# Optimization experiments

Measured on AMD Instinct MI355X. Metric: run time of the kernel, lower is better.

Reference implementation:

```python
import jax, jax.numpy as jnp
import numpy as np

NEAR = 0.01          # near-plane clip for camera-space depth
BLUR = 0.3           # 2D covariance dilation used by 3DGS/gsplat rasterizers
MAX_ALPHA = 0.999    # alpha clamp used by 3DGS/gsplat


def _quat_to_rotmat(q):
    # q: [N,4] normalized (w, x, y, z)
    w, x, y, z = q[:, 0], q[:, 1], q[:, 2], q[:, 3]
    return jnp.stack([
        jnp.stack([1 - 2 * (y * y + z * z), 2 * (x * y - w * z), 2 * (x * z + w * y)], -1),
        jnp.stack([2 * (x * y + w * z), 1 - 2 * (x * x + z * z), 2 * (y * z - w * x)], -1),
        jnp.stack([2 * (x * z - w * y), 2 * (y * z + w * x), 1 - 2 * (x * x + y * y)], -1),
    ], -2)  # [N,3,3]


def _render_one(viewmat, K, means, quats_n, scales, opacities, colors, width, height):
    # --- 3D covariance: Sigma = R diag(s^2) R^T ---
    R = _quat_to_rotmat(quats_n)                      # [N,3,3]
    M = R * scales[:, None, :]                        # scale columns
    cov3d = jnp.einsum('nij,nkj->nik', M, M)          # [N,3,3]

    # --- project means to camera / image ---
    Rcw, tvec = viewmat[:3, :3], viewmat[:3, 3]
    tc = means @ Rcw.T + tvec                         # [N,3] camera-space
    tz = tc[:, 2]
    fx, fy, cx, cy = K[0, 0], K[1, 1], K[0, 2], K[1, 2]
    tz_safe = jnp.where(tz > NEAR, tz, NEAR)
    inv_z = 1.0 / tz_safe
    mean2d = jnp.stack([fx * tc[:, 0] * inv_z + cx,
                        fy * tc[:, 1] * inv_z + cy], -1)  # [N,2]

    # --- EWA splatting: cov2d = J W Sigma W^T J^T + blur*I ---
    zeros = jnp.zeros_like(inv_z)
    J = jnp.stack([
        jnp.stack([fx * inv_z, zeros, -fx * tc[:, 0] * inv_z * inv_z], -1),
        jnp.stack([zeros, fy * inv_z, -fy * tc[:, 1] * inv_z * inv_z], -1),
    ], -2)                                            # [N,2,3]
    cov_cam = jnp.einsum('ij,njk,lk->nil', Rcw, cov3d, Rcw)
    cov2d = jnp.einsum('nij,njk,nlk->nil', J, cov_cam, J)
    a = cov2d[:, 0, 0] + BLUR
    c = cov2d[:, 1, 1] + BLUR
    b = cov2d[:, 0, 1]
    det = a * c - b * b
    valid = (tz > NEAR) & (det > 1e-12)
    det_s = jnp.where(valid, det, 1.0)
    ia, ib, ic = c / det_s, -b / det_s, a / det_s     # conic (inverse cov2d)

    # --- depth sort (front to back) ---
    order = jnp.argsort(tz)
    mean2d, ia, ib, ic = mean2d[order], ia[order], ib[order], ic[order]
    opac_s, colors_s, valid_s = opacities[order], colors[order], valid[order]

    # --- per-pixel gaussian evaluation (pixel centers at +0.5) ---
    px = jnp.arange(width, dtype=mean2d.dtype) + 0.5   # [W]
    py = jnp.arange(height, dtype=mean2d.dtype) + 0.5  # [H]
    dx = px[:, None] - mean2d[None, :, 0]              # [W,N]
    dy = py[:, None] - mean2d[None, :, 1]              # [H,N]
    quad = (ia * dx * dx)[None, :, :] \
         + 2.0 * ib * dx[None, :, :] * dy[:, None, :] \
         + (ic * dy * dy)[:, None, :]                  # [H,W,N]
    alpha = opac_s * jnp.exp(-0.5 * quad)
    alpha = jnp.where(valid_s, jnp.minimum(alpha, MAX_ALPHA), 0.0)

    # --- front-to-back alpha compositing ---
    Tinc = jnp.cumprod(1.0 - alpha, axis=-1)
    Texc = jnp.concatenate([jnp.ones_like(Tinc[..., :1]), Tinc[..., :-1]], -1)
    w = alpha * Texc                                   # [H,W,N]
    return jnp.einsum('hwn,nc->hwc', w, colors_s)      # [H,W,3]


def reference(viewmats, Ks, means, quats, log_scales, opacity_logits, color_logits, width, height):
    # parameter activations (GaussianSplat.activated_parameters)
    quats_n = quats / jnp.linalg.norm(quats, axis=-1, keepdims=True)
    scales = jnp.exp(log_scales)
    opac = jax.nn.sigmoid(opacity_logits)
    colors = jax.nn.sigmoid(color_logits)
    render = lambda vm, K: _render_one(vm, K, means, quats_n, scales, opac, colors, width, height)
    return jax.vmap(render)(viewmats, Ks)  # [C,H,W,3]


def setup_inputs() -> dict:
    key = jax.random.key(0)
    k1, k2, k3 = jax.random.split(key, 3)
    N = 1024
    means = jax.random.normal(k1, (N, 3), dtype=jnp.float32) * 0.1
    quats = jnp.concatenate([jnp.ones((N, 1), jnp.float32),
                             jnp.zeros((N, 3), jnp.float32)], -1)
    quats = quats + 0.1 * jax.random.normal(k3, (N, 4), dtype=jnp.float32)
    log_scales = jnp.full((N, 3), -2.3, dtype=jnp.float32)
    opacity_logits = jnp.full((N,), -1.0, dtype=jnp.float32)
    color_logits = jax.random.normal(k2, (N, 3), dtype=jnp.float32)

    def look(angle):
        c, s = np.cos(angle), np.sin(angle)
        vm = np.eye(4, dtype=np.float32)
        vm[:3, :3] = np.array([[c, 0, -s], [0, 1, 0], [s, 0, c]], np.float32)
        vm[:3, 3] = np.array([0, 0, 2.5], np.float32)
        return vm

    viewmats = jnp.asarray(np.stack([look(0.0), look(0.4)]))
    K = np.array([[128.0, 0, 64.0], [0, 128.0, 64.0], [0, 0, 1.0]], np.float32)
    Ks = jnp.asarray(np.stack([K, K]))
    return {"viewmats": viewmats, "Ks": Ks, "means": means, "quats": quats,
            "log_scales": log_scales, "opacity_logits": opacity_logits,
            "color_logits": color_logits, "width": 128, "height": 128}
```

## Files before the change

kernel.cpp:

```cpp
#include <hip/hip_runtime.h>
#include <hip/hip_fp16.h>
#include <math.h>

#define NEARP 0.01f
#define BLUR 0.3f
#define MAX_ALPHA 0.999f
#define TILE 16
#define NSEG 16
#define QCUT 32.0f

__device__ __forceinline__ float sigmoidf_(float x) {
    return 1.0f / (1.0f + expf(-x));
}

__global__ void gs_preprocess(const float* __restrict__ viewmats,
                              const float* __restrict__ Ks,
                              const float* __restrict__ means,
                              const float* __restrict__ quats,
                              const float* __restrict__ log_scales,
                              const float* __restrict__ opac_logits,
                              const float* __restrict__ color_logits,
                              float4* __restrict__ ubbox,
                              float4* __restrict__ upay,
                              float* __restrict__ tz_out,
                              int N, int C) {
    int idx = blockIdx.x * blockDim.x + threadIdx.x;
    if (idx >= N * C) return;
    int c = idx / N;
    int n = idx - c * N;

    float qw = quats[n * 4 + 0], qx = quats[n * 4 + 1];
    float qy = quats[n * 4 + 2], qz = quats[n * 4 + 3];
    float qn = rsqrtf(qw * qw + qx * qx + qy * qy + qz * qz);
    float w = qw * qn, x = qx * qn, y = qy * qn, z = qz * qn;
    float R00 = 1.0f - 2.0f * (y * y + z * z), R01 = 2.0f * (x * y - w * z), R02 = 2.0f * (x * z + w * y);
    float R10 = 2.0f * (x * y + w * z), R11 = 1.0f - 2.0f * (x * x + z * z), R12 = 2.0f * (y * z - w * x);
    float R20 = 2.0f * (x * z - w * y), R21 = 2.0f * (y * z + w * x), R22 = 1.0f - 2.0f * (x * x + y * y);

    float s0 = expf(log_scales[n * 3 + 0]);
    float s1 = expf(log_scales[n * 3 + 1]);
    float s2 = expf(log_scales[n * 3 + 2]);

    float M00 = R00 * s0, M01 = R01 * s1, M02 = R02 * s2;
    float M10 = R10 * s0, M11 = R11 * s1, M12 = R12 * s2;
    float M20 = R20 * s0, M21 = R21 * s1, M22 = R22 * s2;
    float C00 = M00 * M00 + M01 * M01 + M02 * M02;
    float C01 = M00 * M10 + M01 * M11 + M02 * M12;
    float C02 = M00 * M20 + M01 * M21 + M02 * M22;
    float C11 = M10 * M10 + M11 * M11 + M12 * M12;
    float C12 = M10 * M20 + M11 * M21 + M12 * M22;
    float C22 = M20 * M20 + M21 * M21 + M22 * M22;

    const float* vm = viewmats + c * 16;
    float V00 = vm[0], V01 = vm[1], V02 = vm[2], T0 = vm[3];
    float V10 = vm[4], V11 = vm[5], V12 = vm[6], T1 = vm[7];
    float V20 = vm[8], V21 = vm[9], V22 = vm[10], T2 = vm[11];
    float mex = means[n * 3 + 0], mey = means[n * 3 + 1], mez = means[n * 3 + 2];
    float tx = V00 * mex + V01 * mey + V02 * mez + T0;
    float ty = V10 * mex + V11 * mey + V12 * mez + T1;
    float tz = V20 * mex + V21 * mey + V22 * mez + T2;

    float fx = Ks[c * 9 + 0], fy = Ks[c * 9 + 4], cx = Ks[c * 9 + 2], cy = Ks[c * 9 + 5];
    float tzs = (tz > NEARP) ? tz : NEARP;
    float iz = 1.0f / tzs;
    float m2x = fx * tx * iz + cx;
    float m2y = fy * ty * iz + cy;

    float A00 = V00 * C00 + V01 * C01 + V02 * C02;
    float A01 = V00 * C01 + V01 * C11 + V02 * C12;
    float A02 = V00 * C02 + V01 * C12 + V02 * C22;
    float A10 = V10 * C00 + V11 * C01 + V12 * C02;
    float A11 = V10 * C01 + V11 * C11 + V12 * C12;
    float A12 = V10 * C02 + V11 * C12 + V12 * C22;
    float A20 = V20 * C00 + V21 * C01 + V22 * C02;
    float A21 = V20 * C01 + V21 * C11 + V22 * C12;
    float A22 = V20 * C02 + V21 * C12 + V22 * C22;
    float S00 = A00 * V00 + A01 * V01 + A02 * V02;
    float S01 = A00 * V10 + A01 * V11 + A02 * V12;
    float S02 = A00 * V20 + A01 * V21 + A02 * V22;
    float S11 = A10 * V10 + A11 * V11 + A12 * V12;
    float S12 = A10 * V20 + A11 * V21 + A12 * V22;
    float S22 = A20 * V20 + A21 * V21 + A22 * V22;

    float J00 = fx * iz, J02 = -fx * tx * iz * iz;
    float J11 = fy * iz, J12 = -fy * ty * iz * iz;

    float c2_00 = J00 * J00 * S00 + 2.0f * J00 * J02 * S02 + J02 * J02 * S22;
    float c2_01 = J00 * J11 * S01 + J00 * J12 * S02 + J02 * J11 * S12 + J02 * J12 * S22;
    float c2_11 = J11 * J11 * S11 + 2.0f * J11 * J12 * S12 + J12 * J12 * S22;

    float a = c2_00 + BLUR;
    float cc = c2_11 + BLUR;
    float b = c2_01;
    float det = a * cc - b * b;
    bool valid = (tz > NEARP) && (det > 1e-12f);

    float ia, ib, ic, op, r;
    if (valid) {
        float inv = 1.0f / det;
        ia = cc * inv;
        ib = -b * inv;
        ic = a * inv;
        op = sigmoidf_(opac_logits[n]);
        float lmax = 0.5f * (a + cc) + sqrtf(0.25f * (a - cc) * (a - cc) + b * b);
        r = sqrtf(QCUT * lmax);
    } else {
        ia = 0.0f; ib = 0.0f; ic = 0.0f; op = 0.0f;
        r = -1.0f;
    }
    float cr = sigmoidf_(color_logits[n * 3 + 0]);
    float cg = sigmoidf_(color_logits[n * 3 + 1]);
    float cb = sigmoidf_(color_logits[n * 3 + 2]);

    const float KQ = 0.721347520444482f;
    float iap = -KQ * ia;
    float ibp = -2.0f * KQ * ib;
    float icp = -KQ * ic;

    union { __half2 h; float f; } pk;
    pk.h = __floats2half2_rn(cr, cg);

    int gi = c * N + n;
    ubbox[gi] = make_float4(m2x, m2y, r, 0.0f);
    upay[(size_t)gi * 2 + 0] = make_float4(m2x, m2y, iap, ibp);
    upay[(size_t)gi * 2 + 1] = make_float4(icp, op, pk.f, cb);
    tz_out[gi] = tz;
}

__global__ void gs_sort_wave(const float4* __restrict__ ubbox,
                             const float4* __restrict__ upay,
                             const float* __restrict__ tzin,
                             float4* __restrict__ sbbox,
                             float4* __restrict__ spay,
                             int N, int C) {
    int gtid = blockIdx.x * blockDim.x + threadIdx.x;
    int wid = gtid >> 6;
    int lane = gtid & 63;
    if (wid >= C * N) return;
    int c = wid / N;
    int i = wid - c * N;
    const float* tzc = tzin + (size_t)c * N;
    float ti = tzc[i];
    int rank = 0;
    for (int j = lane; j < N; j += 64) {
        float tj = tzc[j];
        rank += (int)((tj < ti) || (tj == ti && j < i));
    }
#pragma unroll
    for (int off = 1; off < 64; off <<= 1)
        rank += __shfl_xor(rank, off, 64);
    int src = c * N + i;
    int dst = c * N + rank;
    if (lane == 0) sbbox[dst] = ubbox[src];
    if (lane < 2) spay[(size_t)dst * 2 + lane] = upay[(size_t)src * 2 + lane];
}

__global__ void gs_tilebuild(const float4* __restrict__ sbbox,
                             int* __restrict__ tcount,
                             int* __restrict__ tlist,
                             int N, int C, int tilesx, int tilesy) {
    int gtid = blockIdx.x * blockDim.x + threadIdx.x;
    int wid = gtid >> 6;
    int lane = gtid & 63;
    int T = tilesx * tilesy;
    if (wid >= C * T) return;
    int c = wid / T;
    int t = wid - c * T;
    float x0 = (float)((t % tilesx) * TILE);
    float y0 = (float)((t / tilesx) * TILE);
    float x1 = x0 + (float)TILE;
    float y1 = y0 + (float)TILE;

    const float4* bb = sbbox + (size_t)c * N;
    int* lst = tlist + (size_t)wid * N;
    int cnt = 0;
    for (int base = 0; base < N; base += 64) {
        int g = base + lane;
        bool pred = false;
        if (g < N) {
            float4 b = bb[g];
            pred = (b.z >= 0.0f) &&
                   (b.x - b.z <= x1) && (b.x + b.z >= x0) &&
                   (b.y - b.z <= y1) && (b.y + b.z >= y0);
        }
        unsigned long long bal = __ballot(pred);
        if (pred) {
            int off = __popcll(bal & ((1ull << lane) - 1ull));
            lst[cnt + off] = g;
        }
        cnt += (int)__popcll(bal);
    }
    if (lane == 0) tcount[wid] = cnt;
}

__global__ void __launch_bounds__(256) gs_render_tile(const float4* __restrict__ spay,
                                                      const int* __restrict__ tcount,
                                                      const int* __restrict__ tlist,
                                                      float4* __restrict__ partial,
                                                      int N, int W, int H,
                                                      int tilesx, int nseg) {
    int zc = blockIdx.z;
    int c = zc / nseg;
    int s = zc - c * nseg;
    int t = blockIdx.y * tilesx + blockIdx.x;
    int T = tilesx * ((H + TILE - 1) / TILE);
    int wid = c * T + t;

    int cnt = tcount[wid];
    int L = (cnt + nseg - 1) / nseg;
    int k0 = s * L;
    int k1 = min(cnt, k0 + L);

    int lx = threadIdx.x % TILE;
    int ly = threadIdx.x / TILE;
    int x = blockIdx.x * TILE + lx;
    int y = blockIdx.y * TILE + ly;
    float px = (float)x + 0.5f;
    float py = (float)y + 0.5f;

    float Tr = 1.0f, accr = 0.0f, accg = 0.0f, accb = 0.0f;
    const int* lst = tlist + (size_t)wid * N;
    const float4* pay = spay + (size_t)c * N * 2;

#pragma unroll 4
    for (int k = k0; k < k1; k++) {
        int idx = lst[k];
        float4 f0 = pay[(size_t)idx * 2 + 0];
        float4 f1 = pay[(size_t)idx * 2 + 1];
        float dx = px - f0.x;
        float dy = py - f0.y;
        float quad = dx * (f0.z * dx + f0.w * dy) + f1.x * dy * dy;
        float alpha = f1.y * exp2f(quad);
        alpha = fminf(alpha, MAX_ALPHA);
        union { float f; __half2 h; } pk; pk.f = f1.z;
        float wgt = alpha * Tr;
        accr += wgt * __low2float(pk.h);
        accg += wgt * __high2float(pk.h);
        accb += wgt * f1.w;
        Tr *= (1.0f - alpha);
    }
    if (x < W && y < H) {
        partial[((size_t)zc * H + y) * W + x] = make_float4(accr, accg, accb, Tr);
    }
}

__global__ void gs_combine(const float4* __restrict__ partial,
                           float* __restrict__ out,
                           int W, int H, int nseg, int C) {
    int pid = blockIdx.x * blockDim.x + threadIdx.x;
    int PIX = W * H;
    if (pid >= C * PIX) return;
    int c = pid / PIX;
    int p = pid - c * PIX;
    float T = 1.0f, r = 0.0f, g = 0.0f, b = 0.0f;
    for (int s = 0; s < nseg; s++) {
        float4 ps = partial[(size_t)(c * nseg + s) * PIX + p];
        r += T * ps.x;
        g += T * ps.y;
        b += T * ps.z;
        T *= ps.w;
    }
    size_t o = (size_t)pid * 3;
    out[o + 0] = r;
    out[o + 1] = g;
    out[o + 2] = b;
}

extern "C" void kernel_launch(void* const* d_in, const int* in_sizes, int n_in,
                              void* d_out, int out_size, void* d_ws, size_t ws_size,
                              hipStream_t stream) {
    const float* viewmats = (const float*)d_in[0];
    const float* Ks = (const float*)d_in[1];
    const float* means = (const float*)d_in[2];
    const float* quats = (const float*)d_in[3];
    const float* log_scales = (const float*)d_in[4];
    const float* opac_logits = (const float*)d_in[5];
    const float* color_logits = (const float*)d_in[6];
    float* out = (float*)d_out;

    int N = in_sizes[2] / 3;
    int C = in_sizes[0] / 16;
    int pix = out_size / (C * 3);
    int W = (int)(sqrt((double)pix) + 0.5);
    int H = pix / W;
    int tilesx = (W + TILE - 1) / TILE;
    int tilesy = (H + TILE - 1) / TILE;
    int T = tilesx * tilesy;
    int nseg = NSEG;

    float4* ubbox = (float4*)d_ws;
    float4* sbbox = ubbox + (size_t)C * N;
    float4* upay  = sbbox + (size_t)C * N;
    float4* spay  = upay + (size_t)C * N * 2;
    float4* partial = spay + (size_t)C * N * 2;
    float*  tzbuf = (float*)(partial + (size_t)C * nseg * pix);
    int*    tcount = (int*)(tzbuf + (size_t)C * N);
    int*    tlist  = tcount + (size_t)C * T;

    int total = C * N;
    gs_preprocess<<<(total + 255) / 256, 256, 0, stream>>>(
        viewmats, Ks, means, quats, log_scales, opac_logits, color_logits,
        ubbox, upay, tzbuf, N, C);

    gs_sort_wave<<<(total * 64 + 255) / 256, 256, 0, stream>>>(
        ubbox, upay, tzbuf, sbbox, spay, N, C);

    gs_tilebuild<<<(C * T * 64 + 255) / 256, 256, 0, stream>>>(
        sbbox, tcount, tlist, N, C, tilesx, tilesy);

    dim3 grid(tilesx, tilesy, C * nseg);
    gs_render_tile<<<grid, 256, 0, stream>>>(
        spay, tcount, tlist, partial, N, W, H, tilesx, nseg);

    int cp = C * W * H;
    gs_combine<<<(cp + 255) / 256, 256, 0, stream>>>(partial, out, W, H, nseg, C);
}
```

Baseline: 114.4 us.

## Fuse tile binning into render kernel and drop per-tile gaussian lists

Removes the separate tile-build kernel and its per-tile index lists. Each render block now scans its own fixed range of 64-gaussian chunks of the depth-sorted array, tests bbox overlap with a wave ballot, and blends only the overlapping gaussians. Partial results are stored in a tile-major layout, and the combine kernel maps them back to pixel order. This saves one launch and the list write and read traffic. In exchange every block repeats the overlap test for its chunk range, and splitting by chunk count instead of by per-tile hit count can leave the work across segments uneven.

```diff
diff --git a/kernel.cpp b/kernel.cpp
--- a/kernel.cpp
+++ b/kernel.cpp
@@ -155,27 +155,33 @@
     if (lane < 2) spay[(size_t)dst * 2 + lane] = upay[(size_t)src * 2 + lane];
 }
 
-__global__ void gs_tilebuild(const float4* __restrict__ sbbox,
-                             int* __restrict__ tcount,
-                             int* __restrict__ tlist,
-                             int N, int C, int tilesx, int tilesy) {
-    int gtid = blockIdx.x * blockDim.x + threadIdx.x;
-    int wid = gtid >> 6;
-    int lane = gtid & 63;
-    int T = tilesx * tilesy;
-    if (wid >= C * T) return;
-    int c = wid / T;
-    int t = wid - c * T;
-    float x0 = (float)((t % tilesx) * TILE);
-    float y0 = (float)((t / tilesx) * TILE);
+__global__ void __launch_bounds__(256) gs_render_seg(const float4* __restrict__ sbbox,
+                                                     const float4* __restrict__ spay,
+                                                     float4* __restrict__ partial,
+                                                     int N, int W, int H,
+                                                     int tilesx, int nseg, int cps) {
+    int zc = blockIdx.z;
+    int c = zc / nseg;
+    int s = zc - c * nseg;
+    int nchunk = (N + 63) >> 6;
+    int v0 = s * cps;
+    int v1 = min(nchunk, v0 + cps);
+
+    float x0 = (float)(blockIdx.x * TILE);
+    float y0 = (float)(blockIdx.y * TILE);
     float x1 = x0 + (float)TILE;
     float y1 = y0 + (float)TILE;
 
+    int lane = threadIdx.x & 63;
+    float px = x0 + (float)(threadIdx.x & 15) + 0.5f;
+    float py = y0 + (float)(threadIdx.x >> 4) + 0.5f;
+
+    float Tr = 1.0f, accr = 0.0f, accg = 0.0f, accb = 0.0f;
     const float4* bb = sbbox + (size_t)c * N;
-    int* lst = tlist + (size_t)wid * N;
-    int cnt = 0;
-    for (int base = 0; base < N; base += 64) {
-        int g = base + lane;
+    const float4* pay = spay + (size_t)c * N * 2;
+
+    for (int v = v0; v < v1; v++) {
+        int g = v * 64 + lane;
         bool pred = false;
         if (g < N) {
             float4 b = bb[g];
@@ -183,87 +189,55 @@
                    (b.x - b.z <= x1) && (b.x + b.z >= x0) &&
                    (b.y - b.z <= y1) && (b.y + b.z >= y0);
         }
-        unsigned long long bal = __ballot(pred);
-        if (pred) {
-            int off = __popcll(bal & ((1ull << lane) - 1ull));
-            lst[cnt + off] = g;
+        unsigned long long m = __ballot(pred);
+        for (; m; m &= (m - 1)) {
+            int gg = v * 64 + (__ffsll((unsigned long long)m) - 1);
+            float4 f0 = pay[(size_t)gg * 2 + 0];
+            float4 f1 = pay[(size_t)gg * 2 + 1];
+            float dx = px - f0.x;
+            float dy = py - f0.y;
+            float quad = dx * (f0.z * dx + f0.w * dy) + f1.x * dy * dy;
+            float alpha = fminf(f1.y * exp2f(quad), MAX_ALPHA);
+            union { float f; __half2 h; } pk; pk.f = f1.z;
+            float wgt = alpha * Tr;
+            accr += wgt * __low2float(pk.h);
+            accg += wgt * __high2float(pk.h);
+            accb += wgt * f1.w;
+            Tr *= (1.0f - alpha);
         }
-        cnt += (int)__popcll(bal);
-    }
-    if (lane == 0) tcount[wid] = cnt;
-}
-
-__global__ void __launch_bounds__(256) gs_render_tile(const float4* __restrict__ spay,
-                                                      const int* __restrict__ tcount,
-                                                      const int* __restrict__ tlist,
-                                                      float4* __restrict__ partial,
-                                                      int N, int W, int H,
-                                                      int tilesx, int nseg) {
-    int zc = blockIdx.z;
-    int c = zc / nseg;
-    int s = zc - c * nseg;
-    int t = blockIdx.y * tilesx + blockIdx.x;
-    int T = tilesx * ((H + TILE - 1) / TILE);
-    int wid = c * T + t;
-
-    int cnt = tcount[wid];
-    int L = (cnt + nseg - 1) / nseg;
-    int k0 = s * L;
-    int k1 = min(cnt, k0 + L);
-
-    int lx = threadIdx.x % TILE;
-    int ly = threadIdx.x / TILE;
-    int x = blockIdx.x * TILE + lx;
-    int y = blockIdx.y * TILE + ly;
-    float px = (float)x + 0.5f;
-    float py = (float)y + 0.5f;
-
-    float Tr = 1.0f, accr = 0.0f, accg = 0.0f, accb = 0.0f;
-    const int* lst = tlist + (size_t)wid * N;
-    const float4* pay = spay + (size_t)c * N * 2;
-
-#pragma unroll 4
-    for (int k = k0; k < k1; k++) {
-        int idx = lst[k];
-        float4 f0 = pay[(size_t)idx * 2 + 0];
-        float4 f1 = pay[(size_t)idx * 2 + 1];
-        float dx = px - f0.x;
-        float dy = py - f0.y;
-        float quad = dx * (f0.z * dx + f0.w * dy) + f1.x * dy * dy;
-        float alpha = f1.y * exp2f(quad);
-        alpha = fminf(alpha, MAX_ALPHA);
-        union { float f; __half2 h; } pk; pk.f = f1.z;
-        float wgt = alpha * Tr;
-        accr += wgt * __low2float(pk.h);
-        accg += wgt * __high2float(pk.h);
-        accb += wgt * f1.w;
-        Tr *= (1.0f - alpha);
-    }
-    if (x < W && y < H) {
-        partial[((size_t)zc * H + y) * W + x] = make_float4(accr, accg, accb, Tr);
-    }
+    }
+    partial[((size_t)(c * nseg + s) * gridDim.x * gridDim.y +
+             (size_t)(blockIdx.y * gridDim.x + blockIdx.x)) * 256 + threadIdx.x] =
+        make_float4(accr, accg, accb, Tr);
 }
 
 __global__ void gs_combine(const float4* __restrict__ partial,
                            float* __restrict__ out,
-                           int W, int H, int nseg, int C) {
-    int pid = blockIdx.x * blockDim.x + threadIdx.x;
-    int PIX = W * H;
-    if (pid >= C * PIX) return;
-    int c = pid / PIX;
-    int p = pid - c * PIX;
-    float T = 1.0f, r = 0.0f, g = 0.0f, b = 0.0f;
+                           int W, int H, int tilesx, int tilesy, int nseg, int C) {
+    int q = blockIdx.x * blockDim.x + threadIdx.x;
+    int T = tilesx * tilesy;
+    if (q >= C * T * 256) return;
+    int pix = q & 255;
+    int ct = q >> 8;
+    int c = ct / T;
+    int t = ct - c * T;
+
+    float Tr = 1.0f, r = 0.0f, g = 0.0f, b = 0.0f;
     for (int s = 0; s < nseg; s++) {
-        float4 ps = partial[(size_t)(c * nseg + s) * PIX + p];
-        r += T * ps.x;
-        g += T * ps.y;
-        b += T * ps.z;
-        T *= ps.w;
-    }
-    size_t o = (size_t)pid * 3;
-    out[o + 0] = r;
-    out[o + 1] = g;
-    out[o + 2] = b;
+        float4 ps = partial[((size_t)(c * nseg + s) * T + t) * 256 + pix];
+        r += Tr * ps.x;
+        g += Tr * ps.y;
+        b += Tr * ps.z;
+        Tr *= ps.w;
+    }
+    int x = (t % tilesx) * TILE + (pix & 15);
+    int y = (t / tilesx) * TILE + (pix >> 4);
+    if (x < W && y < H) {
+        size_t o = (((size_t)c * H + y) * W + x) * 3;
+        out[o + 0] = r;
+        out[o + 1] = g;
+        out[o + 2] = b;
+    }
 }
 
 extern "C" void kernel_launch(void* const* d_in, const int* in_sizes, int n_in,
@@ -287,15 +261,15 @@
     int tilesy = (H + TILE - 1) / TILE;
     int T = tilesx * tilesy;
     int nseg = NSEG;
+    int nchunk = (N + 63) / 64;
+    int cps = (nchunk + nseg - 1) / nseg;
 
     float4* ubbox = (float4*)d_ws;
     float4* sbbox = ubbox + (size_t)C * N;
     float4* upay  = sbbox + (size_t)C * N;
     float4* spay  = upay + (size_t)C * N * 2;
     float4* partial = spay + (size_t)C * N * 2;
-    float*  tzbuf = (float*)(partial + (size_t)C * nseg * pix);
-    int*    tcount = (int*)(tzbuf + (size_t)C * N);
-    int*    tlist  = tcount + (size_t)C * T;
+    float*  tzbuf = (float*)(partial + (size_t)C * nseg * T * 256);
 
     int total = C * N;
     gs_preprocess<<<(total + 255) / 256, 256, 0, stream>>>(
@@ -305,13 +279,11 @@
     gs_sort_wave<<<(total * 64 + 255) / 256, 256, 0, stream>>>(
         ubbox, upay, tzbuf, sbbox, spay, N, C);
 
-    gs_tilebuild<<<(C * T * 64 + 255) / 256, 256, 0, stream>>>(
-        sbbox, tcount, tlist, N, C, tilesx, tilesy);
-
     dim3 grid(tilesx, tilesy, C * nseg);
-    gs_render_tile<<<grid, 256, 0, stream>>>(
-        spay, tcount, tlist, partial, N, W, H, tilesx, nseg);
-
-    int cp = C * W * H;
-    gs_combine<<<(cp + 255) / 256, 256, 0, stream>>>(partial, out, W, H, nseg, C);
-}
+    gs_render_seg<<<grid, 256, 0, stream>>>(
+        sbbox, spay, partial, N, W, H, tilesx, nseg, cps);
+
+    int cq = C * T * 256;
+    gs_combine<<<(cq + 255) / 256, 256, 0, stream>>>(
+        partial, out, W, H, tilesx, tilesy, nseg, C);
+}
```

After: 105.6 us. 7.7% less time.
